# Kernel tuning notes

Measured on AMD Instinct MI355X. Metric: run time of the kernel, lower is better.

## Reference

```python
import jax, jax.numpy as jnp
import numpy as np

MODES = 128
WIDTH = 128
L_SEG = 20
M_CHEB = 8


def _cft_mag(x):
    # x: [B, C, N] real. Faithful port of vectorized_batched_cft_decomposed
    # (L=20 segments, M=8 Chebyshev nodes), restricted to the first MODES
    # frequencies (the only ones consumed downstream). Returns mean-|CFT|
    # over channels: [B, MODES]. Output is detached in the original code.
    n = x.shape[-1]
    t = jnp.linspace(0.0, 1.0, n)
    freqs = jnp.arange(MODES, dtype=jnp.float32)  # rfftfreq(n, d=1/n)[:MODES]
    seg_len = 1.0 / L_SEG
    a = jnp.linspace(0.0, 1.0, L_SEG + 1)[:-1]  # [L] segment starts
    k = jnp.arange(M_CHEB, dtype=jnp.float32)
    nodes = -jnp.cos((2.0 * k + 1.0) * jnp.pi / (2.0 * M_CHEB))  # [M]
    T = jnp.cos(k[:, None] * jnp.arccos(nodes)[None, :])  # [M(k), M(node)]
    w_prime = freqs * (2.0 * jnp.pi * seg_len / 2.0)  # [F]
    exp_q = jnp.exp(-1j * nodes[:, None] * w_prime[None, :])  # [M, F]
    cheb_w = (T @ exp_q) * (seg_len / 2.0)  # [M, F] complex
    shift = jnp.exp(-1j * 2.0 * jnp.pi * freqs[None, :] * a[:, None])  # [L, F]
    W = shift[:, None, :] * cheb_w[None, :, :]  # [L, M, F]
    # quadrature sample points and linear interpolation from the grid t
    t_seg = a[:, None] + seg_len / 2.0 * (nodes[None, :] + 1.0)  # [L, M]
    right = jnp.minimum(jnp.searchsorted(t, t_seg.reshape(-1)), n - 1).reshape(L_SEG, M_CHEB)
    left = jnp.maximum(right - 1, 0)
    tl, tr = t[left], t[right]
    denom = jnp.where(tr - tl == 0.0, 1.0, tr - tl)
    w_r = (t_seg - tl) / denom
    w_l = 1.0 - w_r
    sig = w_l[None, None] * x[:, :, left] + w_r[None, None] * x[:, :, right]  # [B,C,L,M]
    spec = jnp.einsum('bclm,lmf->bcf', sig.astype(jnp.complex64), W)  # [B,C,F]
    spec = jax.lax.stop_gradient(spec)  # .detach() in the original
    return jnp.mean(jnp.abs(spec), axis=1)  # [B, MODES]


def _forward(x, fc0_W, fc0_b, gate_W, gate_b, wA_re, wA_im, wB_re, wB_im,
             conv_W, conv_b, fc1_W, fc1_b, fc2_W, fc2_b):
    B, N, _ = x.shape
    grid = jnp.broadcast_to(jnp.linspace(0.0, 1.0, N)[None, :, None], (B, N, 1))
    h = jnp.concatenate([x, grid], axis=-1) @ fc0_W.T + fc0_b  # [B,N,W]
    h = h.transpose(0, 2, 1)  # [B,W,N]
    n_f = N // 2 + 1
    for i in range(4):
        mag = _cft_mag(h)  # [B, MODES], detached
        gate = jax.nn.sigmoid(mag @ gate_W[i].T + gate_b[i])  # [B, W]
        # weights1 = gate*A + (1-gate)*B, then the original einsum
        # 'bix,bioy->box' sums weights over the mode axis y; fold that sum
        # into the (in,out) matrices first.
        wA = (wA_re[i] + 1j * wA_im[i]).sum(-1)  # [in, out]
        wB = (wB_re[i] + 1j * wB_im[i]).sum(-1)
        Wg = gate[:, None, :] * wA[None] + (1.0 - gate[:, None, :]) * wB[None]  # [B,in,out]
        h_ft = jnp.fft.rfft(h)  # [B,W,n_f]
        out_modes = jnp.einsum('bif,bio->bof', h_ft[:, :, :MODES], Wg)
        out_ft = jnp.zeros((B, WIDTH, n_f), jnp.complex64).at[:, :, :MODES].set(out_modes)
        x1 = jnp.fft.irfft(out_ft, n=N)  # [B,W,N]
        x2 = jnp.einsum('bcn,oc->bon', h, conv_W[i]) + conv_b[i][None, :, None]
        h = x1 + x2
        if i < 3:
            h = jax.nn.gelu(h, approximate=False)
    h = h.transpose(0, 2, 1)  # [B,N,W]
    h = jax.nn.gelu(h @ fc1_W.T + fc1_b, approximate=False)
    return h @ fc2_W.T + fc2_b  # [B,N,1]


def setup_inputs() -> dict:
    key = jax.random.key(0)
    ks = jax.random.split(key, 16)
    B, N = 64, 4096
    scale = 1.0 / (WIDTH * WIDTH)
    d = {}
    d['x'] = jax.random.normal(ks[0], (B, N, 1), jnp.float32)
    d['fc0_W'] = jax.random.normal(ks[1], (WIDTH, 2), jnp.float32) * 0.1
    d['fc0_b'] = jnp.zeros((WIDTH,), jnp.float32)
    d['gate_W'] = jax.random.normal(ks[2], (4, WIDTH, MODES), jnp.float32) * 0.05
    d['gate_b'] = jnp.zeros((4, WIDTH), jnp.float32)
    d['wA_re'] = jax.random.uniform(ks[3], (4, WIDTH, WIDTH, MODES), jnp.float32) * scale
    d['wA_im'] = jax.random.uniform(ks[4], (4, WIDTH, WIDTH, MODES), jnp.float32) * scale
    d['wB_re'] = jax.random.uniform(ks[5], (4, WIDTH, WIDTH, MODES), jnp.float32) * scale
    d['wB_im'] = jax.random.uniform(ks[6], (4, WIDTH, WIDTH, MODES), jnp.float32) * scale
    d['conv_W'] = jax.random.normal(ks[7], (4, WIDTH, WIDTH), jnp.float32) * 0.05
    d['conv_b'] = jnp.zeros((4, WIDTH), jnp.float32)
    d['fc1_W'] = jax.random.normal(ks[8], (128, WIDTH), jnp.float32) * 0.05
    d['fc1_b'] = jnp.zeros((128,), jnp.float32)
    d['fc2_W'] = jax.random.normal(ks[9], (1, 128), jnp.float32) * 0.05
    d['fc2_b'] = jnp.zeros((1,), jnp.float32)
    return d


def reference(x, fc0_W, fc0_b, gate_W, gate_b, wA_re, wA_im, wB_re, wB_im,
              conv_W, conv_b, fc1_W, fc1_b, fc2_W, fc2_b):
    return _forward(x, fc0_W, fc0_b, gate_W, gate_b, wA_re, wA_im, wB_re, wB_im,
                    conv_W, conv_b, fc1_W, fc1_b, fc2_W, fc2_b)
```

## Files before the change

kernel.cpp:

```cpp
#include <hip/hip_runtime.h>
#include <math.h>

#define B_SZ 64
#define WID 128
#define NPT 4096
#define MODES 128
#define LSEG 20
#define MCH 8
#define LM 160

typedef _Float16 half8 __attribute__((ext_vector_type(8)));
typedef float f32x4 __attribute__((ext_vector_type(4)));

#define LO_SCALE 2048.0f
#define LO_INV   (1.0f/2048.0f)

static constexpr size_t BY_F    = 0;
static constexpr size_t BY_wsum = BY_F + 8388608;
static constexpr size_t BY_Wcre = BY_wsum + 1048576;
static constexpr size_t BY_Wcim = BY_Wcre + 81920;
static constexpr size_t BY_wl   = BY_Wcim + 81920;
static constexpr size_t BY_wr   = BY_wl + 1024;
static constexpr size_t BY_li   = BY_wr + 1024;
static constexpr size_t BY_magp = BY_li + 1024;
static constexpr size_t BY_gate = BY_magp + 524288;
static constexpr size_t BY_hh   = BY_gate + 32768;
static constexpr size_t BY_hl   = BY_hh + 67108864;
static constexpr size_t BY_Tfh  = BY_hl + 67108864;
static constexpr size_t BY_Tfl  = BY_Tfh + 2097152;
static constexpr size_t BY_Tih  = BY_Tfl + 2097152;
static constexpr size_t BY_Til  = BY_Tih + 2097152;
static constexpr size_t BY_Xh   = BY_Til + 2097152;
static constexpr size_t BY_Xl   = BY_Xh + 4194304;
static constexpr size_t BY_cWh  = BY_Xl + 4194304;
static constexpr size_t BY_cWl  = BY_cWh + 131072;
static constexpr size_t BY_f1h  = BY_cWl + 131072;
static constexpr size_t BY_f1l  = BY_f1h + 32768;
static constexpr size_t BY_end  = BY_f1l + 32768;

__device__ __forceinline__ float gelu_f(float x){
    return 0.5f*x*(1.0f+erff(x*0.70710678118654752f));
}
__device__ __forceinline__ void split_f16(float v, _Float16& hi, _Float16& lo){
    hi = (_Float16)v;
    lo = (_Float16)((v - (float)hi)*LO_SCALE);
}

__global__ void k_tables(_Float16* __restrict__ Tfh, _Float16* __restrict__ Tfl,
                         _Float16* __restrict__ Tih, _Float16* __restrict__ Til){
    int idx = blockIdx.x*256 + threadIdx.x;
    int n = idx >> 8, k2 = idx & 255;
    int f = k2 >> 1;
    int m = (n*f) & 4095;
    double th = (double)m * (3.14159265358979323846/2048.0);
    double s, c; sincos(th, &s, &c);
    float vf = (k2&1) ? (float)(-s) : (float)c;
    _Float16 h1,l1; split_f16(vf, h1, l1);
    Tfh[(size_t)k2*4096 + n] = h1;
    Tfl[(size_t)k2*4096 + n] = l1;
    float vi;
    if (k2 == 0)      vi = 1.0f;
    else if (k2 == 1) vi = 0.0f;
    else              vi = vf;
    _Float16 h2,l2; split_f16(vi, h2, l2);
    Tih[(size_t)n*256 + k2] = h2;
    Til[(size_t)n*256 + k2] = l2;
}

__global__ void k_cft_tables(float* __restrict__ Wre, float* __restrict__ Wim,
                             float* __restrict__ wl, float* __restrict__ wr,
                             int* __restrict__ li){
    int idx = blockIdx.x*128 + threadIdx.x;
    if (idx >= LM*MODES) return;
    int lm = idx >> 7;  int f = idx & 127;
    int l = lm / MCH, m = lm % MCH;
    const double PI = 3.14159265358979323846;
    double nodes[8], Tm[8];
    #pragma unroll
    for (int j=0;j<8;j++){
        nodes[j] = -cos((2.0*j+1.0)*PI/16.0);
        Tm[j] = cos((double)m * acos(nodes[j]));
    }
    double wp = (double)f * PI * 0.05;
    double cwre=0.0, cwim=0.0;
    #pragma unroll
    for (int j=0;j<8;j++){
        double sj, cj; sincos(nodes[j]*wp, &sj, &cj);
        cwre += Tm[j]*cj;
        cwim -= Tm[j]*sj;
    }
    cwre *= 0.025; cwim *= 0.025;
    int r = (f*l) % 20;
    double sa = 2.0*PI*(double)r/20.0;
    double shre = cos(sa), shim = -sin(sa);
    Wre[lm*128+f] = (float)(shre*cwre - shim*cwim);
    Wim[lm*128+f] = (float)(shre*cwim + shim*cwre);
    if (f == 0){
        double v = (double)l/20.0 + 0.025*(nodes[m]+1.0);
        int rr = (int)ceil(v*4095.0);
        if (rr > 4095) rr = 4095;
        if (rr < 1) rr = 1;
        int le = rr-1;
        double tl = (double)le/4095.0, tr = (double)rr/4095.0;
        double wrv = (v - tl)/(tr - tl);
        li[lm] = le;
        wl[lm] = (float)(1.0 - wrv);
        wr[lm] = (float)wrv;
    }
}

__global__ void k_wsum(const float* __restrict__ wAre, const float* __restrict__ wAim,
                       const float* __restrict__ wBre, const float* __restrict__ wBim,
                       float* __restrict__ out){
    int row  = blockIdx.x*4 + (threadIdx.x>>6);
    int lane = threadIdx.x & 63;
    const float* src = (blockIdx.y==0)?wAre:(blockIdx.y==1)?wAim:(blockIdx.y==2)?wBre:wBim;
    float v = src[(size_t)row*128 + lane] + src[(size_t)row*128 + 64 + lane];
    #pragma unroll
    for (int o=32;o>0;o>>=1) v += __shfl_down(v, o);
    if (lane==0) out[(size_t)blockIdx.y*65536 + row] = v;
}

__global__ void k_wsplit(const float* __restrict__ convW, const float* __restrict__ fc1W,
                         _Float16* __restrict__ cWh, _Float16* __restrict__ cWl,
                         _Float16* __restrict__ f1h, _Float16* __restrict__ f1l){
    int idx = blockIdx.x*256 + threadIdx.x;
    if (idx < 65536){
        _Float16 hi,lo; split_f16(convW[idx], hi, lo);
        cWh[idx]=hi; cWl[idx]=lo;
    } else {
        int j = idx - 65536;
        _Float16 hi,lo; split_f16(fc1W[j], hi, lo);
        f1h[j]=hi; f1l[j]=lo;
    }
}

__global__ void k_h0(const float* __restrict__ x, const float* __restrict__ w0,
                     const float* __restrict__ b0,
                     _Float16* __restrict__ hh, _Float16* __restrict__ hl){
    int idx = blockIdx.x*256 + threadIdx.x;
    int n8 = idx & 511;
    int w  = (idx >> 9) & 127;
    int b  = idx >> 16;
    int n0 = n8*8;
    float w00 = w0[w*2], w01 = w0[w*2+1], bb = b0[w];
    const float* xr = &x[((size_t)b<<12) + n0];
    float4 x0 = *reinterpret_cast<const float4*>(xr);
    float4 x1 = *reinterpret_cast<const float4*>(xr+4);
    float xv[8]={x0.x,x0.y,x0.z,x0.w,x1.x,x1.y,x1.z,x1.w};
    half8 vh, vl;
    #pragma unroll
    for (int q=0;q<8;q++){
        float g = (float)(n0+q) * (1.0f/4095.0f);
        float v = xv[q]*w00 + g*w01 + bb;
        _Float16 hi,lo; split_f16(v,hi,lo);
        vh[q]=hi; vl[q]=lo;
    }
    size_t o = ((size_t)(b*128+w))*4096 + n0;
    *reinterpret_cast<half8*>(&hh[o]) = vh;
    *reinterpret_cast<half8*>(&hl[o]) = vl;
}

__global__ void k_cft(const _Float16* __restrict__ hh, const _Float16* __restrict__ hl,
                      const float* __restrict__ Wre, const float* __restrict__ Wim,
                      const float* __restrict__ wl, const float* __restrict__ wr,
                      const int* __restrict__ li, float* __restrict__ magp){
    int b = blockIdx.x, cg = blockIdx.y;
    int f = threadIdx.x;
    __shared__ float sig[LM];
    __shared__ float swl[LM], swr[LM];
    __shared__ int   sli[LM];
    for (int s=f; s<LM; s+=128){ swl[s]=wl[s]; swr[s]=wr[s]; sli[s]=li[s]; }
    __syncthreads();
    float acc = 0.f;
    for (int cc=0; cc<8; cc++){
        int c = cg*8 + cc;
        const _Float16* rh = hh + ((size_t)(b*128+c))*4096;
        const _Float16* rl = hl + ((size_t)(b*128+c))*4096;
        for (int s=f; s<LM; s+=128){
            int le = sli[s];
            float v0 = (float)rh[le]   + (float)rl[le]*LO_INV;
            float v1 = (float)rh[le+1] + (float)rl[le+1]*LO_INV;
            sig[s] = swl[s]*v0 + swr[s]*v1;
        }
        __syncthreads();
        float re=0.f, im=0.f;
        #pragma unroll 8
        for (int s=0;s<LM;s++){
            float sv = sig[s];
            re = fmaf(sv, Wre[s*128+f], re);
            im = fmaf(sv, Wim[s*128+f], im);
        }
        acc += sqrtf(re*re+im*im);
        __syncthreads();
    }
    magp[(b*16+cg)*128 + f] = acc;
}

__global__ void k_gate(const float* __restrict__ magp, const float* __restrict__ gW,
                       const float* __restrict__ gB, float* __restrict__ gate, int layer){
    int b = blockIdx.x, w = threadIdx.x;
    __shared__ float ms[128];
    float s = 0.f;
    #pragma unroll
    for (int g=0; g<16; g++) s += magp[(b*16+g)*128 + w];
    ms[w] = s * (1.0f/128.0f);
    __syncthreads();
    const float* gwr = gW + ((size_t)layer*128 + w)*128;
    float a = gB[layer*128 + w];
    #pragma unroll 8
    for (int fq=0; fq<128; fq++) a = fmaf(ms[fq], gwr[fq], a);
    gate[b*128+w] = 1.0f/(1.0f+expf(-a));
}

__global__ __launch_bounds__(256) void k_fdft(
        const _Float16* __restrict__ hh, const _Float16* __restrict__ hl,
        const _Float16* __restrict__ Tfh, const _Float16* __restrict__ Tfl,
        float* __restrict__ F){
    __shared__ _Float16 Ah[2][64][40], Al[2][64][40], Bh[2][64][40], Bl[2][64][40];
    int id = blockIdx.x;
    int swz = (id & 7)*64 + (id >> 3);
    int bx = swz & 3, by = swz >> 2;
    int col0 = bx*64, row0 = by*64;
    int tid = threadIdx.x;
    int lane = tid & 63, w = tid >> 6;
    int wr = (w>>1)*32, wc = (w&1)*32;
    int l15 = lane & 15, l4 = lane >> 4;
    f32x4 acc[2][2] = {}; f32x4 acc2[2][2] = {};
    int srow = tid >> 2, sseg = tid & 3;
    const _Float16* pa_h = hh  + (size_t)(row0+srow)*4096 + sseg*8;
    const _Float16* pa_l = hl  + (size_t)(row0+srow)*4096 + sseg*8;
    const _Float16* pb_h = Tfh + (size_t)(col0+srow)*4096 + sseg*8;
    const _Float16* pb_l = Tfl + (size_t)(col0+srow)*4096 + sseg*8;
    half8 Aah,Aal,Abh,Abl, Bah,Bal,Bbh,Bbl;
#define LOADK(sa,sal,sb,sbl,ck) do{ int kk=(ck)*32; \
    sa  = *reinterpret_cast<const half8*>(pa_h + kk); \
    sal = *reinterpret_cast<const half8*>(pa_l + kk); \
    sb  = *reinterpret_cast<const half8*>(pb_h + kk); \
    sbl = *reinterpret_cast<const half8*>(pb_l + kk); }while(0)
#define WRITEK(sa,sal,sb,sbl,buf) do{ \
    *reinterpret_cast<half8*>(&Ah[buf][srow][sseg*8]) = sa; \
    *reinterpret_cast<half8*>(&Al[buf][srow][sseg*8]) = sal; \
    *reinterpret_cast<half8*>(&Bh[buf][srow][sseg*8]) = sb; \
    *reinterpret_cast<half8*>(&Bl[buf][srow][sseg*8]) = sbl; }while(0)
#define MMF(buf) do{ \
    half8 fah[2], fal[2], fbh[2], fbl[2]; \
    _Pragma("unroll") for (int i=0;i<2;i++){ \
        fah[i] = *reinterpret_cast<const half8*>(&Ah[buf][wr + i*16 + l15][l4*8]); \
        fal[i] = *reinterpret_cast<const half8*>(&Al[buf][wr + i*16 + l15][l4*8]); \
        fbh[i] = *reinterpret_cast<const half8*>(&Bh[buf][wc + i*16 + l15][l4*8]); \
        fbl[i] = *reinterpret_cast<const half8*>(&Bl[buf][wc + i*16 + l15][l4*8]); } \
    _Pragma("unroll") for (int i=0;i<2;i++) \
        _Pragma("unroll") for (int j=0;j<2;j++){ \
            acc[i][j]  = __builtin_amdgcn_mfma_f32_16x16x32_f16(fah[i], fbh[j], acc[i][j], 0,0,0); \
            acc2[i][j] = __builtin_amdgcn_mfma_f32_16x16x32_f16(fah[i], fbl[j], acc2[i][j],0,0,0); \
            acc2[i][j] = __builtin_amdgcn_mfma_f32_16x16x32_f16(fal[i], fbh[j], acc2[i][j],0,0,0); } }while(0)
    LOADK(Aah,Aal,Abh,Abl, 0);
    WRITEK(Aah,Aal,Abh,Abl, 0);
    LOADK(Aah,Aal,Abh,Abl, 1);
    LOADK(Bah,Bal,Bbh,Bbl, 2);
    __syncthreads();
    for (int tt = 0; tt < 64; ++tt){
        int t = tt*2;
        MMF(0);
        WRITEK(Aah,Aal,Abh,Abl, 1);
        if (t+3 < 128) LOADK(Aah,Aal,Abh,Abl, t+3);
        __syncthreads();
        MMF(1);
        if (t+2 < 128) WRITEK(Bah,Bal,Bbh,Bbl, 0);
        if (t+4 < 128) LOADK(Bah,Bal,Bbh,Bbl, t+4);
        __syncthreads();
    }
#undef LOADK
#undef WRITEK
#undef MMF
    #pragma unroll
    for (int i=0;i<2;i++)
        #pragma unroll
        for (int j=0;j<2;j++)
            #pragma unroll
            for (int r=0;r<4;r++){
                int row = row0 + wr + i*16 + l4*4 + r;
                int col = col0 + wc + j*16 + l15;
                F[(size_t)row*256 + col] = acc[i][j][r] + acc2[i][j][r]*LO_INV;
            }
}

__global__ __launch_bounds__(256) void k_modemix(const float* __restrict__ F,
        const float* __restrict__ wsum, const float* __restrict__ gate,
        _Float16* __restrict__ Xh, _Float16* __restrict__ Xl, int layer){
    int b = blockIdx.x, og = blockIdx.y;
    __shared__ float Fs[16][256];
    __shared__ float Wa_re[128][8], Wa_im[128][8], Wb_re[128][8], Wb_im[128][8];
    int tid = threadIdx.x;
    for (int e=tid; e<1024; e+=256){
        int i = e>>3, oo = e&7;
        size_t base = ((size_t)layer*128 + i)*128 + og*8 + oo;
        Wa_re[i][oo] = wsum[0*65536 + base];
        Wa_im[i][oo] = wsum[1*65536 + base];
        Wb_re[i][oo] = wsum[2*65536 + base];
        Wb_im[i][oo] = wsum[3*65536 + base];
    }
    int f = tid & 127, half = tid >> 7;
    float pre[4]={},pim[4]={},qre[4]={},qim[4]={};
    for (int i0=0;i0<128;i0+=16){
        for (int e=tid; e<4096; e+=256){
            int ii = e >> 8, k2 = e & 255;
            Fs[ii][k2] = F[((size_t)(b*128 + i0+ii))*256 + k2];
        }
        __syncthreads();
        #pragma unroll
        for (int ii=0; ii<16; ii++){
            float fre = Fs[ii][2*f], fim = Fs[ii][2*f+1];
            int i = i0+ii;
            #pragma unroll
            for (int q=0;q<4;q++){
                int oo = half*4+q;
                float are=Wa_re[i][oo], aim=Wa_im[i][oo];
                float bre=Wb_re[i][oo], bim=Wb_im[i][oo];
                pre[q] = fmaf(fre, are, fmaf(-fim, aim, pre[q]));
                pim[q] = fmaf(fre, aim, fmaf( fim, are, pim[q]));
                qre[q] = fmaf(fre, bre, fmaf(-fim, bim, qre[q]));
                qim[q] = fmaf(fre, bim, fmaf( fim, bre, qim[q]));
            }
        }
        __syncthreads();
    }
    #pragma unroll
    for (int q=0;q<4;q++){
        int o = og*8 + half*4 + q;
        float g = gate[b*128+o];
        float xre = g*pre[q] + (1.f-g)*qre[q];
        float xim = g*pim[q] + (1.f-g)*qim[q];
        float s = (f==0) ? (1.0f/4096.0f) : (2.0f/4096.0f);
        xre *= s; xim *= s;
        if (f==0) xim = 0.f;
        size_t base = ((size_t)(b*128+o))*256 + 2*f;
        _Float16 h1,l1; split_f16(xre,h1,l1); Xh[base]=h1;   Xl[base]=l1;
        _Float16 h2,l2; split_f16(xim,h2,l2); Xh[base+1]=h2; Xl[base+1]=l2;
    }
}

__global__ __launch_bounds__(256) void k_flayer(
    const _Float16* __restrict__ Xh, const _Float16* __restrict__ Xl,
    const _Float16* __restrict__ Tih, const _Float16* __restrict__ Til,
    const _Float16* __restrict__ cWh, const _Float16* __restrict__ cWl,
    const float* __restrict__ convB,
    _Float16* __restrict__ hh, _Float16* __restrict__ hl,
    int layer, int applyGelu){
    __shared__ _Float16 As_h[2][128][40], As_l[2][128][40];
    __shared__ _Float16 Bs_h[2][64][40],  Bs_l[2][64][40];
    int n0 = blockIdx.x*64;
    int b  = blockIdx.y;
    int tid = threadIdx.x, lane = tid & 63, w = tid >> 6;
    int l15 = lane & 15, l4 = lane >> 4;
    int o0 = w*32;
    int aro = tid >> 2, asl = tid & 3;
    int ctc = tid >> 3, ctn = tid & 7;
    int ocp = ((tid >> 6) ^ (tid & 3));
    const _Float16* cA_h = cWh + (size_t)layer*16384 + (size_t)aro*128 + asl*8;
    const _Float16* cA_l = cWl + (size_t)layer*16384 + (size_t)aro*128 + asl*8;
    const _Float16* xA_h = Xh + ((size_t)(b*128 + aro))*256 + asl*8;
    const _Float16* xA_l = Xl + ((size_t)(b*128 + aro))*256 + asl*8;
    const _Float16* hB_h = hh + ((size_t)(b*128 + ctc))*4096 + n0 + ctn*8;
    const _Float16* hB_l = hl + ((size_t)(b*128 + ctc))*4096 + n0 + ctn*8;
    const _Float16* tB_h = Tih + (size_t)(n0 + aro)*256 + asl*8;
    const _Float16* tB_l = Til + (size_t)(n0 + aro)*256 + asl*8;
    f32x4 acc[2][4] = {}; f32x4 acc2[2][4] = {};
    half8 rA[6], rB[6];
#define LOADR(r,ck) do{ \
    if ((ck) < 4){ int kk = (ck)*32; \
        r[0] = *reinterpret_cast<const half8*>(cA_h + kk); \
        r[1] = *reinterpret_cast<const half8*>(cA_l + kk); \
        r[2] = *reinterpret_cast<const half8*>(cA_h + 64*128 + kk); \
        r[3] = *reinterpret_cast<const half8*>(cA_l + 64*128 + kk); \
        r[4] = *reinterpret_cast<const half8*>(hB_h + (size_t)(ck)*32*4096); \
        r[5] = *reinterpret_cast<const half8*>(hB_l + (size_t)(ck)*32*4096); \
    } else { int kk = ((ck)-4)*32; \
        r[0] = *reinterpret_cast<const half8*>(xA_h + kk); \
        r[1] = *reinterpret_cast<const half8*>(xA_l + kk); \
        r[2] = *reinterpret_cast<const half8*>(xA_h + 64*256 + kk); \
        r[3] = *reinterpret_cast<const half8*>(xA_l + 64*256 + kk); \
        r[4] = *reinterpret_cast<const half8*>(tB_h + kk); \
        r[5] = *reinterpret_cast<const half8*>(tB_l + kk); } }while(0)
#define WRITER(r,buf,ck) do{ \
    *reinterpret_cast<half8*>(&As_h[buf][aro][asl*8])    = r[0]; \
    *reinterpret_cast<half8*>(&As_l[buf][aro][asl*8])    = r[1]; \
    *reinterpret_cast<half8*>(&As_h[buf][aro+64][asl*8]) = r[2]; \
    *reinterpret_cast<half8*>(&As_l[buf][aro+64][asl*8]) = r[3]; \
    if ((ck) < 4){ \
        _Pragma("unroll") for (int j2=0;j2<8;j2++){ \
            int n = ctn*8 + j2; \
            Bs_h[buf][n][ocp*8 + (ctc&7)] = r[4][j2]; \
            Bs_l[buf][n][ocp*8 + (ctc&7)] = r[5][j2]; } \
    } else { \
        *reinterpret_cast<half8*>(&Bs_h[buf][aro][asl*8]) = r[4]; \
        *reinterpret_cast<half8*>(&Bs_l[buf][aro][asl*8]) = r[5]; } }while(0)
#define MML(buf,ck) do{ \
    half8 ah[2], al[2], bh[4], bl[4]; \
    _Pragma("unroll") for (int i=0;i<2;i++){ \
        ah[i] = *reinterpret_cast<const half8*>(&As_h[buf][o0+i*16+l15][l4*8]); \
        al[i] = *reinterpret_cast<const half8*>(&As_l[buf][o0+i*16+l15][l4*8]); } \
    if ((ck) < 4){ \
        _Pragma("unroll") for (int j=0;j<4;j++){ \
            int n = j*16 + l15; int sl = (l4 ^ ((n>>3)&3)); \
            bh[j] = *reinterpret_cast<const half8*>(&Bs_h[buf][n][sl*8]); \
            bl[j] = *reinterpret_cast<const half8*>(&Bs_l[buf][n][sl*8]); } \
    } else { \
        _Pragma("unroll") for (int j=0;j<4;j++){ \
            bh[j] = *reinterpret_cast<const half8*>(&Bs_h[buf][j*16+l15][l4*8]); \
            bl[j] = *reinterpret_cast<const half8*>(&Bs_l[buf][j*16+l15][l4*8]); } } \
    _Pragma("unroll") for (int i=0;i<2;i++) \
        _Pragma("unroll") for (int j=0;j<4;j++){ \
            acc[i][j]  = __builtin_amdgcn_mfma_f32_16x16x32_f16(ah[i], bh[j], acc[i][j], 0,0,0); \
            acc2[i][j] = __builtin_amdgcn_mfma_f32_16x16x32_f16(ah[i], bl[j], acc2[i][j],0,0,0); \
            acc2[i][j] = __builtin_amdgcn_mfma_f32_16x16x32_f16(al[i], bh[j], acc2[i][j],0,0,0); } }while(0)
    LOADR(rA, 0);
    WRITER(rA, 0, 0);
    LOADR(rA, 1);
    LOADR(rB, 2);
    __syncthreads();
    #pragma unroll
    for (int tt=0; tt<6; ++tt){
        const int t = 2*tt;
        MML(0, t);
        WRITER(rA, 1, t+1);
        if (t+3 < 12) LOADR(rA, t+3);
        __syncthreads();
        MML(1, t+1);
        if (t+2 < 12) WRITER(rB, 0, t+2);
        if (t+4 < 12) LOADR(rB, t+4);
        __syncthreads();
    }
#undef LOADR
#undef WRITER
#undef MML
    #pragma unroll
    for (int i=0;i<2;i++)
        #pragma unroll
        for (int j=0;j<4;j++)
            #pragma unroll
            for (int r=0;r<4;r++){
                int o = o0 + i*16 + l4*4 + r;
                int n = n0 + j*16 + l15;
                float v = acc[i][j][r] + acc2[i][j][r]*LO_INV + convB[layer*128+o];
                if (applyGelu) v = gelu_f(v);
                _Float16 hi,lo; split_f16(v,hi,lo);
                size_t oi = ((size_t)(b*128+o))*4096 + n;
                hh[oi] = hi; hl[oi] = lo;
            }
}

__global__ __launch_bounds__(256) void k_head(
        const _Float16* __restrict__ hh, const _Float16* __restrict__ hl,
        const _Float16* __restrict__ f1h, const _Float16* __restrict__ f1l,
        const float* __restrict__ fc1b,
        const float* __restrict__ fc2W, const float* __restrict__ fc2b,
        float* __restrict__ out){
    __shared__ _Float16 Bch[64][136], Bcl[64][136];
    __shared__ _Float16 Ash[128][40], Asl[128][40];
    __shared__ float red[16][64];
    int n0 = blockIdx.x*64;
    int b  = blockIdx.y;
    int tid = threadIdx.x, lane = tid & 63, w = tid >> 6;
    int l15 = lane & 15, l4 = lane >> 4;
    int j0 = w*32;
    {
        int c = tid & 127, nh = tid >> 7;
        const _Float16* rh = hh + ((size_t)(b*128+c))*4096 + n0 + nh*32;
        const _Float16* rl = hl + ((size_t)(b*128+c))*4096 + n0 + nh*32;
        #pragma unroll
        for (int j=0;j<4;j++){
            half8 vhv = *reinterpret_cast<const half8*>(rh + j*8);
            half8 vlv = *reinterpret_cast<const half8*>(rl + j*8);
            #pragma unroll
            for (int q=0;q<8;q++){
                int n = nh*32 + j*8 + q;
                Bch[n][c] = vhv[q];
                Bcl[n][c] = vlv[q];
            }
        }
    }
    __syncthreads();
    int so2 = tid >> 2, sseg = tid & 3;
    f32x4 acc[2][4] = {}; f32x4 acc2[2][4] = {};
    for (int k0=0;k0<128;k0+=32){
        #pragma unroll
        for (int p=0;p<2;p++){
            int o = p*64 + so2;
            *reinterpret_cast<half8*>(&Ash[o][sseg*8]) =
                *reinterpret_cast<const half8*>(&f1h[(size_t)o*128 + k0 + sseg*8]);
            *reinterpret_cast<half8*>(&Asl[o][sseg*8]) =
                *reinterpret_cast<const half8*>(&f1l[(size_t)o*128 + k0 + sseg*8]);
        }
        __syncthreads();
        half8 ah[2],al[2],bh[4],bl[4];
        #pragma unroll
        for (int i=0;i<2;i++){
            ah[i] = *reinterpret_cast<const half8*>(&Ash[j0+i*16+l15][l4*8]);
            al[i] = *reinterpret_cast<const half8*>(&Asl[j0+i*16+l15][l4*8]);
        }
        #pragma unroll
        for (int j=0;j<4;j++){
            bh[j] = *reinterpret_cast<const half8*>(&Bch[j*16+l15][k0+l4*8]);
            bl[j] = *reinterpret_cast<const half8*>(&Bcl[j*16+l15][k0+l4*8]);
        }
        #pragma unroll
        for (int i=0;i<2;i++)
            #pragma unroll
            for (int j=0;j<4;j++){
                acc[i][j]  = __builtin_amdgcn_mfma_f32_16x16x32_f16(ah[i], bh[j], acc[i][j], 0,0,0);
                acc2[i][j] = __builtin_amdgcn_mfma_f32_16x16x32_f16(ah[i], bl[j], acc2[i][j],0,0,0);
                acc2[i][j] = __builtin_amdgcn_mfma_f32_16x16x32_f16(al[i], bh[j], acc2[i][j],0,0,0);
            }
        __syncthreads();
    }
    float part[4];
    #pragma unroll
    for (int j=0;j<4;j++) part[j] = 0.f;
    #pragma unroll
    for (int i=0;i<2;i++){
        #pragma unroll
        for (int r=0;r<4;r++){
            int jj = j0 + i*16 + l4*4 + r;
            float b1 = fc1b[jj];
            float w2 = fc2W[jj];
            #pragma unroll
            for (int j=0;j<4;j++){
                float v = acc[i][j][r] + acc2[i][j][r]*LO_INV + b1;
                part[j] = fmaf(w2, gelu_f(v), part[j]);
            }
        }
    }
    #pragma unroll
    for (int j=0;j<4;j++) red[w*4+l4][j*16+l15] = part[j];
    __syncthreads();
    if (tid < 64){
        float s = fc2b[0];
        #pragma unroll
        for (int r=0;r<16;r++) s += red[r][tid];
        out[((size_t)b<<12) + n0 + tid] = s;
    }
}

extern "C" void kernel_launch(void* const* d_in, const int* in_sizes, int n_in,
                              void* d_out, int out_size, void* d_ws, size_t ws_size,
                              hipStream_t stream) {
    const float* x     = (const float*)d_in[0];
    const float* fc0W  = (const float*)d_in[1];
    const float* fc0b  = (const float*)d_in[2];
    const float* gateW = (const float*)d_in[3];
    const float* gateB = (const float*)d_in[4];
    const float* wAre  = (const float*)d_in[5];
    const float* wAim  = (const float*)d_in[6];
    const float* wBre  = (const float*)d_in[7];
    const float* wBim  = (const float*)d_in[8];
    const float* convW = (const float*)d_in[9];
    const float* convB = (const float*)d_in[10];
    const float* fc1W  = (const float*)d_in[11];
    const float* fc1b  = (const float*)d_in[12];
    const float* fc2W  = (const float*)d_in[13];
    const float* fc2b  = (const float*)d_in[14];
    float* out = (float*)d_out;
    char*  wsb = (char*)d_ws;

    float* F    = (float*)(wsb + BY_F);
    float* wsum = (float*)(wsb + BY_wsum);
    float* Wcre = (float*)(wsb + BY_Wcre);
    float* Wcim = (float*)(wsb + BY_Wcim);
    float* wl   = (float*)(wsb + BY_wl);
    float* wr   = (float*)(wsb + BY_wr);
    int*   li   = (int*)(wsb + BY_li);
    float* magp = (float*)(wsb + BY_magp);
    float* gate = (float*)(wsb + BY_gate);
    _Float16* hh  = (_Float16*)(wsb + BY_hh);
    _Float16* hl  = (_Float16*)(wsb + BY_hl);
    _Float16* Tfh = (_Float16*)(wsb + BY_Tfh);
    _Float16* Tfl = (_Float16*)(wsb + BY_Tfl);
    _Float16* Tih = (_Float16*)(wsb + BY_Tih);
    _Float16* Til = (_Float16*)(wsb + BY_Til);
    _Float16* Xh  = (_Float16*)(wsb + BY_Xh);
    _Float16* Xl  = (_Float16*)(wsb + BY_Xl);
    _Float16* cWh = (_Float16*)(wsb + BY_cWh);
    _Float16* cWl = (_Float16*)(wsb + BY_cWl);
    _Float16* f1h = (_Float16*)(wsb + BY_f1h);
    _Float16* f1l = (_Float16*)(wsb + BY_f1l);

    k_tables<<<4096, 256, 0, stream>>>(Tfh, Tfl, Tih, Til);
    k_cft_tables<<<160, 128, 0, stream>>>(Wcre, Wcim, wl, wr, li);
    k_wsum<<<dim3(16384,4), 256, 0, stream>>>(wAre, wAim, wBre, wBim, wsum);
    k_wsplit<<<320, 256, 0, stream>>>(convW, fc1W, cWh, cWl, f1h, f1l);
    k_h0<<<16384, 256, 0, stream>>>(x, fc0W, fc0b, hh, hl);

    for (int layer=0; layer<4; layer++){
        k_cft<<<dim3(64,16), 128, 0, stream>>>(hh, hl, Wcre, Wcim, wl, wr, li, magp);
        k_gate<<<64, 128, 0, stream>>>(magp, gateW, gateB, gate, layer);
        k_fdft<<<512, 256, 0, stream>>>(hh, hl, Tfh, Tfl, F);
        k_modemix<<<dim3(64,16), 256, 0, stream>>>(F, wsum, gate, Xh, Xl, layer);
        k_flayer<<<dim3(64,64), 256, 0, stream>>>(Xh, Xl, Tih, Til, cWh, cWl, convB,
                                                  hh, hl, layer, layer<3 ? 1:0);
    }
    k_head<<<dim3(64,64), 256, 0, stream>>>(hh, hl, f1h, f1l, fc1b, fc2W, fc2b, out);
    (void)in_sizes; (void)n_in; (void)out_size; (void)ws_size;
}
```

Measured before the change: 1.390 ms.

## Use 128x128 tiles with split-K forward DFT and larger inverse-layer tiles

The forward DFT GEMM now uses 128x128 output tiles and splits the 4096-long K dimension into four chunks, writing partial results to four F buffers that the mode-mix kernel sums while loading. The inverse/conv layer GEMM widens its N tile from 64 to 128, giving each wave a 64x64 sub-tile, and both kernels get launch bounds that ask for two blocks per CU. The aim is more data reuse per shared-memory load and better MFMA density. In exchange it uses more registers and shared memory per block, and it adds a larger workspace plus extra reads of partial sums in mode-mix.

```diff
diff --git a/kernel.cpp b/kernel.cpp
--- a/kernel.cpp
+++ b/kernel.cpp
@@ -16,7 +16,7 @@
 #define LO_INV   (1.0f/2048.0f)
 
 static constexpr size_t BY_F    = 0;
-static constexpr size_t BY_wsum = BY_F + 8388608;
+static constexpr size_t BY_wsum = BY_F + 33554432;
 static constexpr size_t BY_Wcre = BY_wsum + 1048576;
 static constexpr size_t BY_Wcim = BY_Wcre + 81920;
 static constexpr size_t BY_wl   = BY_Wcim + 81920;
@@ -213,80 +213,88 @@
     gate[b*128+w] = 1.0f/(1.0f+expf(-a));
 }
 
-__global__ __launch_bounds__(256) void k_fdft(
+__global__ __launch_bounds__(256, 2) void k_fdft(
         const _Float16* __restrict__ hh, const _Float16* __restrict__ hl,
         const _Float16* __restrict__ Tfh, const _Float16* __restrict__ Tfl,
-        float* __restrict__ F){
-    __shared__ _Float16 Ah[2][64][40], Al[2][64][40], Bh[2][64][40], Bl[2][64][40];
-    int id = blockIdx.x;
-    int swz = (id & 7)*64 + (id >> 3);
-    int bx = swz & 3, by = swz >> 2;
-    int col0 = bx*64, row0 = by*64;
-    int tid = threadIdx.x;
-    int lane = tid & 63, w = tid >> 6;
-    int wr = (w>>1)*32, wc = (w&1)*32;
+        float* __restrict__ Fp){
+    __shared__ _Float16 Ah[2][128][38], Al[2][128][38], Bh[2][128][38], Bl[2][128][38];
+    int bid = blockIdx.x;
+    int swz = (bid & 7)*64 + (bid >> 3);
+    int rowb = swz & 63, colb = (swz >> 6) & 1, ks = swz >> 7;
+    int row0 = rowb*128, col0 = colb*128, kbase = ks*1024;
+    int tid = threadIdx.x, lane = tid & 63, w = tid >> 6;
     int l15 = lane & 15, l4 = lane >> 4;
-    f32x4 acc[2][2] = {}; f32x4 acc2[2][2] = {};
-    int srow = tid >> 2, sseg = tid & 3;
-    const _Float16* pa_h = hh  + (size_t)(row0+srow)*4096 + sseg*8;
-    const _Float16* pa_l = hl  + (size_t)(row0+srow)*4096 + sseg*8;
-    const _Float16* pb_h = Tfh + (size_t)(col0+srow)*4096 + sseg*8;
-    const _Float16* pb_l = Tfl + (size_t)(col0+srow)*4096 + sseg*8;
-    half8 Aah,Aal,Abh,Abl, Bah,Bal,Bbh,Bbl;
-#define LOADK(sa,sal,sb,sbl,ck) do{ int kk=(ck)*32; \
-    sa  = *reinterpret_cast<const half8*>(pa_h + kk); \
-    sal = *reinterpret_cast<const half8*>(pa_l + kk); \
-    sb  = *reinterpret_cast<const half8*>(pb_h + kk); \
-    sbl = *reinterpret_cast<const half8*>(pb_l + kk); }while(0)
-#define WRITEK(sa,sal,sb,sbl,buf) do{ \
-    *reinterpret_cast<half8*>(&Ah[buf][srow][sseg*8]) = sa; \
-    *reinterpret_cast<half8*>(&Al[buf][srow][sseg*8]) = sal; \
-    *reinterpret_cast<half8*>(&Bh[buf][srow][sseg*8]) = sb; \
-    *reinterpret_cast<half8*>(&Bl[buf][srow][sseg*8]) = sbl; }while(0)
+    int wo = (w>>1)*64, wc = (w&1)*64;
+    f32x4 acc[4][4] = {}; f32x4 acc2[4][4] = {};
+    int aro = tid >> 2, asl = tid & 3;
+    const _Float16* pa_h = hh  + (size_t)(row0+aro)*4096 + kbase + asl*8;
+    const _Float16* pa_l = hl  + (size_t)(row0+aro)*4096 + kbase + asl*8;
+    const _Float16* pb_h = Tfh + (size_t)(col0+aro)*4096 + kbase + asl*8;
+    const _Float16* pb_l = Tfl + (size_t)(col0+aro)*4096 + kbase + asl*8;
+    half8 rA[8], rB[8];
+#define LOADK(r,ck) do{ size_t kk = (size_t)(ck)*32; \
+    r[0] = *reinterpret_cast<const half8*>(pa_h + kk); \
+    r[1] = *reinterpret_cast<const half8*>(pa_l + kk); \
+    r[2] = *reinterpret_cast<const half8*>(pa_h + (size_t)64*4096 + kk); \
+    r[3] = *reinterpret_cast<const half8*>(pa_l + (size_t)64*4096 + kk); \
+    r[4] = *reinterpret_cast<const half8*>(pb_h + kk); \
+    r[5] = *reinterpret_cast<const half8*>(pb_l + kk); \
+    r[6] = *reinterpret_cast<const half8*>(pb_h + (size_t)64*4096 + kk); \
+    r[7] = *reinterpret_cast<const half8*>(pb_l + (size_t)64*4096 + kk); }while(0)
+#define WRITEK(r,buf) do{ \
+    *reinterpret_cast<half8*>(&Ah[buf][aro][asl*8])    = r[0]; \
+    *reinterpret_cast<half8*>(&Al[buf][aro][asl*8])    = r[1]; \
+    *reinterpret_cast<half8*>(&Ah[buf][aro+64][asl*8]) = r[2]; \
+    *reinterpret_cast<half8*>(&Al[buf][aro+64][asl*8]) = r[3]; \
+    *reinterpret_cast<half8*>(&Bh[buf][aro][asl*8])    = r[4]; \
+    *reinterpret_cast<half8*>(&Bl[buf][aro][asl*8])    = r[5]; \
+    *reinterpret_cast<half8*>(&Bh[buf][aro+64][asl*8]) = r[6]; \
+    *reinterpret_cast<half8*>(&Bl[buf][aro+64][asl*8]) = r[7]; }while(0)
 #define MMF(buf) do{ \
-    half8 fah[2], fal[2], fbh[2], fbl[2]; \
-    _Pragma("unroll") for (int i=0;i<2;i++){ \
-        fah[i] = *reinterpret_cast<const half8*>(&Ah[buf][wr + i*16 + l15][l4*8]); \
-        fal[i] = *reinterpret_cast<const half8*>(&Al[buf][wr + i*16 + l15][l4*8]); \
-        fbh[i] = *reinterpret_cast<const half8*>(&Bh[buf][wc + i*16 + l15][l4*8]); \
-        fbl[i] = *reinterpret_cast<const half8*>(&Bl[buf][wc + i*16 + l15][l4*8]); } \
-    _Pragma("unroll") for (int i=0;i<2;i++) \
-        _Pragma("unroll") for (int j=0;j<2;j++){ \
-            acc[i][j]  = __builtin_amdgcn_mfma_f32_16x16x32_f16(fah[i], fbh[j], acc[i][j], 0,0,0); \
-            acc2[i][j] = __builtin_amdgcn_mfma_f32_16x16x32_f16(fah[i], fbl[j], acc2[i][j],0,0,0); \
-            acc2[i][j] = __builtin_amdgcn_mfma_f32_16x16x32_f16(fal[i], fbh[j], acc2[i][j],0,0,0); } }while(0)
-    LOADK(Aah,Aal,Abh,Abl, 0);
-    WRITEK(Aah,Aal,Abh,Abl, 0);
-    LOADK(Aah,Aal,Abh,Abl, 1);
-    LOADK(Bah,Bal,Bbh,Bbl, 2);
+    half8 bh[4], bl[4]; \
+    _Pragma("unroll") for (int j=0;j<4;j++){ \
+        bh[j] = *reinterpret_cast<const half8*>(&Bh[buf][wc + j*16 + l15][l4*8]); \
+        bl[j] = *reinterpret_cast<const half8*>(&Bl[buf][wc + j*16 + l15][l4*8]); } \
+    _Pragma("unroll") for (int i=0;i<4;i++){ \
+        half8 ah = *reinterpret_cast<const half8*>(&Ah[buf][wo + i*16 + l15][l4*8]); \
+        half8 al = *reinterpret_cast<const half8*>(&Al[buf][wo + i*16 + l15][l4*8]); \
+        _Pragma("unroll") for (int j=0;j<4;j++){ \
+            acc[i][j]  = __builtin_amdgcn_mfma_f32_16x16x32_f16(ah, bh[j], acc[i][j], 0,0,0); \
+            acc2[i][j] = __builtin_amdgcn_mfma_f32_16x16x32_f16(ah, bl[j], acc2[i][j],0,0,0); \
+            acc2[i][j] = __builtin_amdgcn_mfma_f32_16x16x32_f16(al, bh[j], acc2[i][j],0,0,0); } } }while(0)
+    LOADK(rA, 0);
+    WRITEK(rA, 0);
+    LOADK(rA, 1);
+    LOADK(rB, 2);
     __syncthreads();
-    for (int tt = 0; tt < 64; ++tt){
+    for (int tt = 0; tt < 16; ++tt){
         int t = tt*2;
         MMF(0);
-        WRITEK(Aah,Aal,Abh,Abl, 1);
-        if (t+3 < 128) LOADK(Aah,Aal,Abh,Abl, t+3);
+        WRITEK(rA, 1);
+        if (t+3 < 32) LOADK(rA, t+3);
         __syncthreads();
         MMF(1);
-        if (t+2 < 128) WRITEK(Bah,Bal,Bbh,Bbl, 0);
-        if (t+4 < 128) LOADK(Bah,Bal,Bbh,Bbl, t+4);
+        if (t+2 < 32) WRITEK(rB, 0);
+        if (t+4 < 32) LOADK(rB, t+4);
         __syncthreads();
     }
 #undef LOADK
 #undef WRITEK
 #undef MMF
-    #pragma unroll
-    for (int i=0;i<2;i++)
-        #pragma unroll
-        for (int j=0;j<2;j++)
+    float* Fo = Fp + (size_t)ks*2097152;
+    #pragma unroll
+    for (int i=0;i<4;i++)
+        #pragma unroll
+        for (int j=0;j<4;j++)
             #pragma unroll
             for (int r=0;r<4;r++){
-                int row = row0 + wr + i*16 + l4*4 + r;
+                int row = row0 + wo + i*16 + l4*4 + r;
                 int col = col0 + wc + j*16 + l15;
-                F[(size_t)row*256 + col] = acc[i][j][r] + acc2[i][j][r]*LO_INV;
+                Fo[(size_t)row*256 + col] = acc[i][j][r] + acc2[i][j][r]*LO_INV;
             }
 }
 
-__global__ __launch_bounds__(256) void k_modemix(const float* __restrict__ F,
+__global__ __launch_bounds__(256) void k_modemix(const float* __restrict__ Fp,
         const float* __restrict__ wsum, const float* __restrict__ gate,
         _Float16* __restrict__ Xh, _Float16* __restrict__ Xl, int layer){
     int b = blockIdx.x, og = blockIdx.y;
@@ -306,7 +314,8 @@
     for (int i0=0;i0<128;i0+=16){
         for (int e=tid; e<4096; e+=256){
             int ii = e >> 8, k2 = e & 255;
-            Fs[ii][k2] = F[((size_t)(b*128 + i0+ii))*256 + k2];
+            size_t idx = ((size_t)(b*128 + i0+ii))*256 + k2;
+            Fs[ii][k2] = Fp[idx] + Fp[idx+2097152] + Fp[idx+4194304] + Fp[idx+6291456];
         }
         __syncthreads();
         #pragma unroll
@@ -341,20 +350,20 @@
     }
 }
 
-__global__ __launch_bounds__(256) void k_flayer(
+__global__ __launch_bounds__(256, 2) void k_flayer(
     const _Float16* __restrict__ Xh, const _Float16* __restrict__ Xl,
     const _Float16* __restrict__ Tih, const _Float16* __restrict__ Til,
     const _Float16* __restrict__ cWh, const _Float16* __restrict__ cWl,
     const float* __restrict__ convB,
     _Float16* __restrict__ hh, _Float16* __restrict__ hl,
     int layer, int applyGelu){
-    __shared__ _Float16 As_h[2][128][40], As_l[2][128][40];
-    __shared__ _Float16 Bs_h[2][64][40],  Bs_l[2][64][40];
-    int n0 = blockIdx.x*64;
+    __shared__ _Float16 Ah[2][128][38], Al[2][128][38], Bh[2][128][38], Bl[2][128][38];
+    int n0 = blockIdx.x*128;
     int b  = blockIdx.y;
     int tid = threadIdx.x, lane = tid & 63, w = tid >> 6;
     int l15 = lane & 15, l4 = lane >> 4;
-    int o0 = w*32;
+    int wo = (w>>1)*64, wn = (w&1)*64;
+    f32x4 acc[4][4] = {}; f32x4 acc2[4][4] = {};
     int aro = tid >> 2, asl = tid & 3;
     int ctc = tid >> 3, ctn = tid & 7;
     int ocp = ((tid >> 6) ^ (tid & 3));
@@ -366,55 +375,61 @@
     const _Float16* hB_l = hl + ((size_t)(b*128 + ctc))*4096 + n0 + ctn*8;
     const _Float16* tB_h = Tih + (size_t)(n0 + aro)*256 + asl*8;
     const _Float16* tB_l = Til + (size_t)(n0 + aro)*256 + asl*8;
-    f32x4 acc[2][4] = {}; f32x4 acc2[2][4] = {};
-    half8 rA[6], rB[6];
+    half8 rA[8], rB[8];
 #define LOADR(r,ck) do{ \
-    if ((ck) < 4){ int kk = (ck)*32; \
+    if ((ck) < 4){ size_t kk = (size_t)(ck)*32; \
         r[0] = *reinterpret_cast<const half8*>(cA_h + kk); \
         r[1] = *reinterpret_cast<const half8*>(cA_l + kk); \
         r[2] = *reinterpret_cast<const half8*>(cA_h + 64*128 + kk); \
         r[3] = *reinterpret_cast<const half8*>(cA_l + 64*128 + kk); \
         r[4] = *reinterpret_cast<const half8*>(hB_h + (size_t)(ck)*32*4096); \
         r[5] = *reinterpret_cast<const half8*>(hB_l + (size_t)(ck)*32*4096); \
-    } else { int kk = ((ck)-4)*32; \
+        r[6] = *reinterpret_cast<const half8*>(hB_h + (size_t)(ck)*32*4096 + 64); \
+        r[7] = *reinterpret_cast<const half8*>(hB_l + (size_t)(ck)*32*4096 + 64); \
+    } else { size_t kk = (size_t)((ck)-4)*32; \
         r[0] = *reinterpret_cast<const half8*>(xA_h + kk); \
         r[1] = *reinterpret_cast<const half8*>(xA_l + kk); \
         r[2] = *reinterpret_cast<const half8*>(xA_h + 64*256 + kk); \
         r[3] = *reinterpret_cast<const half8*>(xA_l + 64*256 + kk); \
         r[4] = *reinterpret_cast<const half8*>(tB_h + kk); \
-        r[5] = *reinterpret_cast<const half8*>(tB_l + kk); } }while(0)
+        r[5] = *reinterpret_cast<const half8*>(tB_l + kk); \
+        r[6] = *reinterpret_cast<const half8*>(tB_h + 64*256 + kk); \
+        r[7] = *reinterpret_cast<const half8*>(tB_l + 64*256 + kk); } }while(0)
 #define WRITER(r,buf,ck) do{ \
-    *reinterpret_cast<half8*>(&As_h[buf][aro][asl*8])    = r[0]; \
-    *reinterpret_cast<half8*>(&As_l[buf][aro][asl*8])    = r[1]; \
-    *reinterpret_cast<half8*>(&As_h[buf][aro+64][asl*8]) = r[2]; \
-    *reinterpret_cast<half8*>(&As_l[buf][aro+64][asl*8]) = r[3]; \
+    *reinterpret_cast<half8*>(&Ah[buf][aro][asl*8])    = r[0]; \
+    *reinterpret_cast<half8*>(&Al[buf][aro][asl*8])    = r[1]; \
+    *reinterpret_cast<half8*>(&Ah[buf][aro+64][asl*8]) = r[2]; \
+    *reinterpret_cast<half8*>(&Al[buf][aro+64][asl*8]) = r[3]; \
     if ((ck) < 4){ \
         _Pragma("unroll") for (int j2=0;j2<8;j2++){ \
-            int n = ctn*8 + j2; \
-            Bs_h[buf][n][ocp*8 + (ctc&7)] = r[4][j2]; \
-            Bs_l[buf][n][ocp*8 + (ctc&7)] = r[5][j2]; } \
+            int n1 = ctn*8 + j2; \
+            Bh[buf][n1][ocp*8 + (ctc&7)]    = r[4][j2]; \
+            Bl[buf][n1][ocp*8 + (ctc&7)]    = r[5][j2]; \
+            Bh[buf][n1+64][ocp*8 + (ctc&7)] = r[6][j2]; \
+            Bl[buf][n1+64][ocp*8 + (ctc&7)] = r[7][j2]; } \
     } else { \
-        *reinterpret_cast<half8*>(&Bs_h[buf][aro][asl*8]) = r[4]; \
-        *reinterpret_cast<half8*>(&Bs_l[buf][aro][asl*8]) = r[5]; } }while(0)
+        *reinterpret_cast<half8*>(&Bh[buf][aro][asl*8])    = r[4]; \
+        *reinterpret_cast<half8*>(&Bl[buf][aro][asl*8])    = r[5]; \
+        *reinterpret_cast<half8*>(&Bh[buf][aro+64][asl*8]) = r[6]; \
+        *reinterpret_cast<half8*>(&Bl[buf][aro+64][asl*8]) = r[7]; } }while(0)
 #define MML(buf,ck) do{ \
-    half8 ah[2], al[2], bh[4], bl[4]; \
-    _Pragma("unroll") for (int i=0;i<2;i++){ \
-        ah[i] = *reinterpret_cast<const half8*>(&As_h[buf][o0+i*16+l15][l4*8]); \
-        al[i] = *reinterpret_cast<const half8*>(&As_l[buf][o0+i*16+l15][l4*8]); } \
+    half8 bh[4], bl[4]; \
     if ((ck) < 4){ \
         _Pragma("unroll") for (int j=0;j<4;j++){ \
-            int n = j*16 + l15; int sl = (l4 ^ ((n>>3)&3)); \
-            bh[j] = *reinterpret_cast<const half8*>(&Bs_h[buf][n][sl*8]); \
-            bl[j] = *reinterpret_cast<const half8*>(&Bs_l[buf][n][sl*8]); } \
+            int n = wn + j*16 + l15; int sl = (l4 ^ ((n>>3)&3)); \
+            bh[j] = *reinterpret_cast<const half8*>(&Bh[buf][n][sl*8]); \
+            bl[j] = *reinterpret_cast<const half8*>(&Bl[buf][n][sl*8]); } \
     } else { \
         _Pragma("unroll") for (int j=0;j<4;j++){ \
-            bh[j] = *reinterpret_cast<const half8*>(&Bs_h[buf][j*16+l15][l4*8]); \
-            bl[j] = *reinterpret_cast<const half8*>(&Bs_l[buf][j*16+l15][l4*8]); } } \
-    _Pragma("unroll") for (int i=0;i<2;i++) \
+            bh[j] = *reinterpret_cast<const half8*>(&Bh[buf][wn + j*16 + l15][l4*8]); \
+            bl[j] = *reinterpret_cast<const half8*>(&Bl[buf][wn + j*16 + l15][l4*8]); } } \
+    _Pragma("unroll") for (int i=0;i<4;i++){ \
+        half8 ah = *reinterpret_cast<const half8*>(&Ah[buf][wo + i*16 + l15][l4*8]); \
+        half8 al = *reinterpret_cast<const half8*>(&Al[buf][wo + i*16 + l15][l4*8]); \
         _Pragma("unroll") for (int j=0;j<4;j++){ \
-            acc[i][j]  = __builtin_amdgcn_mfma_f32_16x16x32_f16(ah[i], bh[j], acc[i][j], 0,0,0); \
-            acc2[i][j] = __builtin_amdgcn_mfma_f32_16x16x32_f16(ah[i], bl[j], acc2[i][j],0,0,0); \
-            acc2[i][j] = __builtin_amdgcn_mfma_f32_16x16x32_f16(al[i], bh[j], acc2[i][j],0,0,0); } }while(0)
+            acc[i][j]  = __builtin_amdgcn_mfma_f32_16x16x32_f16(ah, bh[j], acc[i][j], 0,0,0); \
+            acc2[i][j] = __builtin_amdgcn_mfma_f32_16x16x32_f16(ah, bl[j], acc2[i][j],0,0,0); \
+            acc2[i][j] = __builtin_amdgcn_mfma_f32_16x16x32_f16(al, bh[j], acc2[i][j],0,0,0); } } }while(0)
     LOADR(rA, 0);
     WRITER(rA, 0, 0);
     LOADR(rA, 1);
@@ -436,13 +451,13 @@
 #undef WRITER
 #undef MML
     #pragma unroll
-    for (int i=0;i<2;i++)
+    for (int i=0;i<4;i++)
         #pragma unroll
         for (int j=0;j<4;j++)
             #pragma unroll
             for (int r=0;r<4;r++){
-                int o = o0 + i*16 + l4*4 + r;
-                int n = n0 + j*16 + l15;
+                int o = wo + i*16 + l4*4 + r;
+                int n = n0 + wn + j*16 + l15;
                 float v = acc[i][j][r] + acc2[i][j][r]*LO_INV + convB[layer*128+o];
                 if (applyGelu) v = gelu_f(v);
                 _Float16 hi,lo; split_f16(v,hi,lo);
@@ -564,7 +579,7 @@
     float* out = (float*)d_out;
     char*  wsb = (char*)d_ws;
 
-    float* F    = (float*)(wsb + BY_F);
+    float* Fp   = (float*)(wsb + BY_F);
     float* wsum = (float*)(wsb + BY_wsum);
     float* Wcre = (float*)(wsb + BY_Wcre);
     float* Wcim = (float*)(wsb + BY_Wcim);
@@ -595,9 +610,9 @@
     for (int layer=0; layer<4; layer++){
         k_cft<<<dim3(64,16), 128, 0, stream>>>(hh, hl, Wcre, Wcim, wl, wr, li, magp);
         k_gate<<<64, 128, 0, stream>>>(magp, gateW, gateB, gate, layer);
-        k_fdft<<<512, 256, 0, stream>>>(hh, hl, Tfh, Tfl, F);
-        k_modemix<<<dim3(64,16), 256, 0, stream>>>(F, wsum, gate, Xh, Xl, layer);
-        k_flayer<<<dim3(64,64), 256, 0, stream>>>(Xh, Xl, Tih, Til, cWh, cWl, convB,
+        k_fdft<<<512, 256, 0, stream>>>(hh, hl, Tfh, Tfl, Fp);
+        k_modemix<<<dim3(64,16), 256, 0, stream>>>(Fp, wsum, gate, Xh, Xl, layer);
+        k_flayer<<<dim3(32,64), 256, 0, stream>>>(Xh, Xl, Tih, Til, cWh, cWl, convB,
                                                   hh, hl, layer, layer<3 ? 1:0);
     }
     k_head<<<dim3(64,64), 256, 0, stream>>>(hh, hl, f1h, f1l, fc1b, fc2W, fc2b, out);
```

Result: slower. 2.702 ms (+94.4%).
